# Performance work log

Measured on AMD Instinct MI355X. Metric: run time of the kernel, lower is better.

## Reference

```python
import jax, jax.numpy as jnp
import numpy as np

B, S, H, D = 4, 2048, 16, 128
E = H * D  # emb_dim = 2048


def setup_inputs() -> dict:
    key = jax.random.key(0)
    ks = jax.random.split(key, 9)
    s_in = 1.0 / np.sqrt(E)
    return {
        "inputs": jax.random.normal(ks[0], (B, S, E), dtype=jnp.float32),
        "Wq": jax.random.normal(ks[1], (E, E), dtype=jnp.float32) * s_in,
        "bq": jnp.zeros((E,), dtype=jnp.float32),
        "Wk": jax.random.normal(ks[2], (E, E), dtype=jnp.float32) * s_in,
        "bk": jnp.zeros((E,), dtype=jnp.float32),
        "Wv": jax.random.normal(ks[3], (E, E), dtype=jnp.float32) * s_in,
        "bv": jnp.zeros((E,), dtype=jnp.float32),
        "Wo": jax.random.normal(ks[4], (E, E), dtype=jnp.float32) * s_in,
        "bo": jnp.zeros((E,), dtype=jnp.float32),
    }


def reference(inputs, Wq, bq, Wk, bk, Wv, bv, Wo, bo):
    b, s, e = inputs.shape
    # QKV projections -> [B, H, S, D]
    q = (inputs @ Wq + bq).reshape(b, s, H, D).transpose(0, 2, 1, 3)
    k = (inputs @ Wk + bk).reshape(b, s, H, D).transpose(0, 2, 1, 3)
    v = (inputs @ Wv + bv).reshape(b, s, H, D).transpose(0, 2, 1, 3)
    scale = 1.0 / jnp.sqrt(jnp.asarray(D, dtype=q.dtype))
    # Scaled dot-product attention (what the blockwise flash loop computes)
    scores = jnp.einsum('bhqd,bhkd->bhqk', q, k) * scale
    probs = jax.nn.softmax(scores, axis=-1)
    attn = jnp.einsum('bhqk,bhkd->bhqd', probs, v)
    attn = attn.transpose(0, 2, 1, 3).reshape(b, s, e)
    return attn @ Wo + bo
```

## Files before the change

kernel.cpp:

```cpp
#include <hip/hip_runtime.h>
#include <hip/hip_bf16.h>
#include <stdint.h>

typedef __bf16 bf16;
typedef float f32x4 __attribute__((ext_vector_type(4)));
typedef bf16 bf16x4 __attribute__((ext_vector_type(4)));
typedef bf16 bf16x8 __attribute__((ext_vector_type(8)));

#define DEV __device__ __forceinline__

DEV void gload16(const void* g, void* l) {
  __builtin_amdgcn_global_load_lds((const __attribute__((address_space(1))) void*)g,
                                   (__attribute__((address_space(3))) void*)l, 16, 0, 0);
}

DEV f32x4 mfma16(bf16x8 a, bf16x8 b, f32x4 c) {
  return __builtin_amdgcn_mfma_f32_16x16x32_bf16(a, b, c, 0, 0, 0);
}

#if __has_builtin(__builtin_amdgcn_exp2f)
DEV float EXP2F(float x) { return __builtin_amdgcn_exp2f(x); }
#else
DEV float EXP2F(float x) { return exp2f(x); }
#endif

static constexpr int Bn = 4, Sn = 2048, Hn = 16, Dn = 128, En = 2048, Mn = 8192;

__global__ void prep(const float* __restrict__ X, bf16* __restrict__ Xb,
                     const float* __restrict__ Wq, const float* __restrict__ Wk,
                     const float* __restrict__ Wv, const float* __restrict__ Wo,
                     bf16* __restrict__ Wqt, bf16* __restrict__ Wkt,
                     bf16* __restrict__ Wvt, bf16* __restrict__ Wot, int n8) {
  __shared__ bf16 t[64][65];
  const int bid = blockIdx.x;
  if (bid < 2048) {
    int i = bid * 256 + threadIdx.x;
    const int stride = 2048 * 256;
    for (int idx = i; idx < n8; idx += stride) {
      const float4* p = (const float4*)(X + (size_t)idx * 8);
      float4 a = p[0], b = p[1];
      bf16x8 o;
      o[0]=(bf16)a.x; o[1]=(bf16)a.y; o[2]=(bf16)a.z; o[3]=(bf16)a.w;
      o[4]=(bf16)b.x; o[5]=(bf16)b.y; o[6]=(bf16)b.z; o[7]=(bf16)b.w;
      *(bf16x8*)(Xb + (size_t)idx * 8) = o;
    }
    return;
  }
  const int q = bid - 2048;
  const int mtx = q >> 10, within = q & 1023;
  const float* W = (mtx == 0) ? Wq : (mtx == 1) ? Wk : (mtx == 2) ? Wv : Wo;
  bf16* Wt = (mtx == 0) ? Wqt : (mtx == 1) ? Wkt : (mtx == 2) ? Wvt : Wot;
  int tx = threadIdx.x & 15, ty = threadIdx.x >> 4;
  int c0 = (within & 31) * 64, r0 = (within >> 5) * 64;
  #pragma unroll
  for (int i = 0; i < 4; ++i) {
    int r = i * 16 + ty;
    float4 v = *(const float4*)&W[(size_t)(r0 + r) * En + c0 + tx * 4];
    t[r][tx*4+0] = (bf16)v.x; t[r][tx*4+1] = (bf16)v.y;
    t[r][tx*4+2] = (bf16)v.z; t[r][tx*4+3] = (bf16)v.w;
  }
  __syncthreads();
  #pragma unroll
  for (int i = 0; i < 4; ++i) {
    int c = i * 16 + ty;
    bf16x4 o;
    #pragma unroll
    for (int j = 0; j < 4; ++j) o[j] = t[tx*4+j][c];
    *(bf16x4*)&Wt[(size_t)(c0 + c) * En + r0 + tx * 4] = o;
  }
}

#define STAGE_A(H, DBUF, KTN) do { \
    const bf16* s_ = A + (size_t)(mbase + (tid >> 2)) * K + (KTN) * 64 + (H) * 32 \
                     + (((tid & 3) ^ ((tid >> 3) & 3)) * 8); \
    gload16(s_, (DBUF) + (H) * 16384 + (w << 10)); \
  } while (0)
#define STAGE_B(H, DBUF, KTN) do { \
    const bf16* s_ = Bt + (size_t)(nbase + (tid >> 2)) * K + (KTN) * 64 + (H) * 32 \
                     + (((tid & 3) ^ ((tid >> 3) & 3)) * 8); \
    gload16(s_, (DBUF) + (H) * 16384 + (w << 10)); \
  } while (0)

template<int OUT_MODE>
__global__ __launch_bounds__(1024, 2) void gemm256(
    const bf16* __restrict__ A, const bf16* __restrict__ Bt,
    const float* __restrict__ b0, const float* __restrict__ b1,
    const float* __restrict__ b2, void* __restrict__ Cout,
    bf16* __restrict__ Vout,
    int M, int N, int K, int sbx, int sby)
{
  __shared__ __align__(16) uint8_t smem[131072];
  const int tid = threadIdx.x, lane = tid & 63, w = tid >> 6;
  const int wm = w >> 2, wn = w & 3;
  const int g = lane >> 4, lr = lane & 15;
  const int gx = (g ^ ((lr >> 1) & 3)) << 4;
  const int lid = blockIdx.x;
  const int xcd = lid & 7, i = lid >> 3;
  const int bx = (xcd & 1) * sbx + (i % sbx);
  const int by = (xcd >> 1) * sby + (i / sbx);
  const int mbase = by * 256, nbase = bx * 256;

  f32x4 acc[4][4] = {};

  STAGE_A(0, smem, 0);
  STAGE_B(0, smem + 65536, 0);
  STAGE_A(1, smem, 0);
  STAGE_B(1, smem + 65536, 0);
  asm volatile("s_waitcnt vmcnt(0)" ::: "memory");
  __builtin_amdgcn_s_barrier();

  const int NKT = K >> 6;
  for (int kt = 0; kt < NKT; ++kt) {
    const int cur = kt & 1;
    uint8_t* Acur = smem + (cur << 15);
    uint8_t* Bcur = smem + 65536 + (cur << 15);
    uint8_t* Anxt = smem + ((cur ^ 1) << 15);
    uint8_t* Bnxt = smem + 65536 + ((cur ^ 1) << 15);
    const bool notlast = (kt + 1 < NKT);

    if (notlast) {
      STAGE_A(0, Anxt, kt + 1);
      STAGE_B(0, Bnxt, kt + 1);
      STAGE_A(1, Anxt, kt + 1);
      STAGE_B(1, Bnxt, kt + 1);
    }

    #pragma unroll
    for (int kh = 0; kh < 2; ++kh) {
      bf16x8 af[4], bfv[4];
      #pragma unroll
      for (int mf = 0; mf < 4; ++mf)
        af[mf] = *(const bf16x8*)(Acur + kh * 16384 + (wm * 64 + mf * 16 + lr) * 64 + gx);
      #pragma unroll
      for (int j = 0; j < 4; ++j)
        bfv[j] = *(const bf16x8*)(Bcur + kh * 16384 + (wn * 64 + j * 16 + lr) * 64 + gx);
      __builtin_amdgcn_s_setprio(1);
      #pragma unroll
      for (int mf = 0; mf < 4; ++mf)
        #pragma unroll
        for (int j = 0; j < 4; ++j)
          acc[mf][j] = mfma16(af[mf], bfv[j], acc[mf][j]);
      __builtin_amdgcn_s_setprio(0);
    }

    asm volatile("s_waitcnt vmcnt(0)" ::: "memory");
    __builtin_amdgcn_s_barrier();
  }

  if constexpr (OUT_MODE == 0) {
    int tsel = nbase >> 11;
    if (tsel == 2) {
      #pragma unroll
      for (int j = 0; j < 4; ++j) {
        int nn = (nbase + wn * 64 + j * 16 + lr) & 2047;
        int h = nn >> 7, d = nn & 127;
        float bv = b2[nn];
        #pragma unroll
        for (int mf = 0; mf < 4; ++mf) {
          int m0 = mbase + wm * 64 + mf * 16 + g * 4;
          int b = m0 >> 11, s0 = m0 & 2047;
          bf16x4 o4;
          #pragma unroll
          for (int r = 0; r < 4; ++r) o4[r] = (bf16)(acc[mf][j][r] + bv);
          *(bf16x4*)&Vout[((size_t)(b * Hn + h) * Dn + d) * Sn + s0] = o4;
        }
      }
    } else {
      const float* bsel = (tsel == 0) ? b0 : b1;
      #pragma unroll
      for (int j = 0; j < 4; ++j) {
        int n = nbase + wn * 64 + j * 16 + lr;
        int nn = n & 2047;
        float bv = bsel[nn];
        int h = nn >> 7, d = nn & 127;
        #pragma unroll
        for (int mf = 0; mf < 4; ++mf) {
          #pragma unroll
          for (int r = 0; r < 4; ++r) {
            int m = mbase + wm * 64 + mf * 16 + g * 4 + r;
            int b = m >> 11, s = m & 2047;
            ((bf16*)Cout)[(size_t)tsel * ((size_t)Mn * En) +
                          ((size_t)(b * Hn + h) * Sn + s) * Dn + d] = (bf16)(acc[mf][j][r] + bv);
          }
        }
      }
    }
  } else {
    #pragma unroll
    for (int j = 0; j < 4; ++j) {
      int n = nbase + wn * 64 + j * 16 + lr;
      float bv = b0[n];
      #pragma unroll
      for (int mf = 0; mf < 4; ++mf) {
        #pragma unroll
        for (int r = 0; r < 4; ++r) {
          int m = mbase + wm * 64 + mf * 16 + g * 4 + r;
          ((float*)Cout)[(size_t)m * N + n] = acc[mf][j][r] + bv;
        }
      }
    }
  }
}

__global__ __launch_bounds__(512, 2) void attn(
    const bf16* __restrict__ Q, const bf16* __restrict__ K,
    const bf16* __restrict__ Vt, bf16* __restrict__ O)
{
  __shared__ __align__(16) uint8_t smem[65536];
  const int tid = threadIdx.x, lane = tid & 63, w = tid >> 6;
  const int g = lane >> 4, lr = lane & 15;
  const int lid = blockIdx.x;
  const int xcd = lid & 7, j = lid >> 3;
  const int bh = xcd * 8 + (j >> 3);
  const int q0 = (j & 7) * 256;
  const size_t hoff = (size_t)bh * Sn * Dn;
  const bf16* Qh = Q + hoff;
  const bf16* Kh = K + hoff;
  const bf16* Vh = Vt + hoff;
  const float SC2 = 0.12751744f;

  #pragma unroll
  for (int it = 0; it < 8; ++it) {
    int cl = it * 512 + tid;
    int row = cl >> 4, cs = cl & 15;
    int cg = cs ^ (row & 7);
    gload16(Qh + (size_t)(q0 + row) * Dn + cg * 8, smem + (it * 512 + (tid & ~63)) * 16);
  }
  __syncthreads();
  bf16x8 qf[2][4];
  #pragma unroll
  for (int nf = 0; nf < 2; ++nf)
    #pragma unroll
    for (int ks = 0; ks < 4; ++ks) {
      int row = w * 32 + nf * 16 + lr;
      qf[nf][ks] = *(const bf16x8*)(smem + row * 256 + (((ks * 4 + g) ^ (row & 7)) << 4));
    }
  __syncthreads();

  const int vd = tid >> 2, vq = tid & 3;
  const bf16* vrow = Vh + (size_t)vd * Sn + (vq >> 1) * 32 + (vq & 1) * 8;

  uint4 u0, u1;
  #pragma unroll
  for (int it = 0; it < 2; ++it) {
    int cl = it * 512 + tid;
    int row = cl >> 4, cs = cl & 15;
    int cg = cs ^ (row & 7);
    gload16(Kh + (size_t)row * Dn + cg * 8, smem + (it * 512 + (tid & ~63)) * 16);
  }
  { const uint4* vs = (const uint4*)vrow; u0 = vs[0]; u1 = vs[2]; }

  f32x4 o[2][8] = {};
  float m2[2] = { -__builtin_inff(), -__builtin_inff() };
  float lrun[2] = { 0.f, 0.f };

  for (int t = 0; t < 32; ++t) {
    const int cur = t & 1;
    uint8_t* Kcur = smem + (cur << 14);
    uint8_t* Knxt = smem + ((cur ^ 1) << 14);
    uint8_t* Vcur = smem + 32768 + (cur << 14);
    asm volatile("s_waitcnt vmcnt(0)" ::: "memory");
    {
      uint8_t* base = Vcur + vd * 128;
      const int sw = vd & 7;
      *(uint4*)(base + (((2 * vq + 0) ^ sw) << 4)) = make_uint4(u0.x, u0.y, u1.x, u1.y);
      *(uint4*)(base + (((2 * vq + 1) ^ sw) << 4)) = make_uint4(u0.z, u0.w, u1.z, u1.w);
    }
    if (t < 31) {
      const int kvn = (t + 1) * 64;
      #pragma unroll
      for (int it = 0; it < 2; ++it) {
        int cl = it * 512 + tid;
        int row = cl >> 4, cs = cl & 15;
        int cg = cs ^ (row & 7);
        gload16(Kh + (size_t)(kvn + row) * Dn + cg * 8,
                Knxt + (it * 512 + (tid & ~63)) * 16);
      }
      const uint4* vs = (const uint4*)(vrow + kvn);
      u0 = vs[0]; u1 = vs[2];
    }
    asm volatile("s_waitcnt lgkmcnt(0)" ::: "memory");
    asm volatile("s_barrier" ::: "memory");

    f32x4 sfr[2][4] = {};
    __builtin_amdgcn_s_setprio(1);
    #pragma unroll
    for (int ks = 0; ks < 4; ++ks) {
      #pragma unroll
      for (int mf = 0; mf < 4; ++mf) {
        int row = mf * 16 + lr;
        bf16x8 kf = *(const bf16x8*)(Kcur + row * 256 + (((ks * 4 + g) ^ (row & 7)) << 4));
        sfr[0][mf] = mfma16(kf, qf[0][ks], sfr[0][mf]);
        sfr[1][mf] = mfma16(kf, qf[1][ks], sfr[1][mf]);
      }
    }
    __builtin_amdgcn_s_setprio(0);

    bf16x8 pa[2][2];
    #pragma unroll
    for (int nf = 0; nf < 2; ++nf) {
      f32x4 a0, a1;
      #pragma unroll
      for (int r = 0; r < 4; ++r) a0[r] = fmaxf(sfr[nf][0][r], sfr[nf][1][r]);
      #pragma unroll
      for (int r = 0; r < 4; ++r) a1[r] = fmaxf(sfr[nf][2][r], sfr[nf][3][r]);
      #pragma unroll
      for (int r = 0; r < 4; ++r) a0[r] = fmaxf(a0[r], a1[r]);
      float mx = fmaxf(fmaxf(a0[0], a0[1]), fmaxf(a0[2], a0[3]));
      mx = fmaxf(mx, __shfl_xor(mx, 16));
      mx = fmaxf(mx, __shfl_xor(mx, 32));
      float pm2 = mx * SC2;
      if (__any(pm2 > m2[nf] + 8.f)) {
        float mnew = fmaxf(m2[nf], pm2);
        float fsc = EXP2F(m2[nf] - mnew);
        m2[nf] = mnew;
        lrun[nf] *= fsc;
        float fv[4];
        #pragma unroll
        for (int r = 0; r < 4; ++r) fv[r] = __shfl(fsc, g * 4 + r);
        #pragma unroll
        for (int df = 0; df < 8; ++df)
          #pragma unroll
          for (int r = 0; r < 4; ++r) o[nf][df][r] *= fv[r];
      }
      const float mc = m2[nf];
      f32x4 p[4];
      #pragma unroll
      for (int mf = 0; mf < 4; ++mf)
        #pragma unroll
        for (int r = 0; r < 4; ++r)
          p[mf][r] = EXP2F(__builtin_fmaf(sfr[nf][mf][r], SC2, -mc));
      f32x4 s0, s1;
      #pragma unroll
      for (int r = 0; r < 4; ++r) s0[r] = p[0][r] + p[1][r];
      #pragma unroll
      for (int r = 0; r < 4; ++r) s1[r] = p[2][r] + p[3][r];
      #pragma unroll
      for (int r = 0; r < 4; ++r) s0[r] += s1[r];
      float ps = (s0[0] + s0[1]) + (s0[2] + s0[3]);
      ps += __shfl_xor(ps, 16);
      ps += __shfl_xor(ps, 32);
      lrun[nf] += ps;
      #pragma unroll
      for (int ks = 0; ks < 2; ++ks) {
        bf16x8 tt;
        #pragma unroll
        for (int i = 0; i < 4; ++i) {
          tt[i]     = (bf16)p[2 * ks][i];
          tt[i + 4] = (bf16)p[2 * ks + 1][i];
        }
        pa[nf][ks] = tt;
      }
    }

    __builtin_amdgcn_s_setprio(1);
    #pragma unroll
    for (int ks = 0; ks < 2; ++ks) {
      #pragma unroll
      for (int df = 0; df < 8; ++df) {
        int row = df * 16 + lr;
        bf16x8 vf = *(const bf16x8*)(Vcur + row * 128 + (((ks * 4 + g) ^ (row & 7)) << 4));
        o[0][df] = mfma16(pa[0][ks], vf, o[0][df]);
        o[1][df] = mfma16(pa[1][ks], vf, o[1][df]);
      }
    }
    __builtin_amdgcn_s_setprio(0);
    asm volatile("s_barrier" ::: "memory");
  }

  const int b = bh >> 4, h = bh & 15;
  #pragma unroll
  for (int nf = 0; nf < 2; ++nf) {
    float inv = 1.f / lrun[nf];
    float iv[4];
    #pragma unroll
    for (int r = 0; r < 4; ++r) iv[r] = __shfl(inv, g * 4 + r);
    #pragma unroll
    for (int df = 0; df < 8; ++df) {
      #pragma unroll
      for (int r = 0; r < 4; ++r) {
        int qrow = q0 + w * 32 + nf * 16 + g * 4 + r;
        int d = df * 16 + lr;
        size_t m = (size_t)b * Sn + qrow;
        O[m * En + h * Dn + d] = (bf16)(o[nf][df][r] * iv[r]);
      }
    }
  }
}

extern "C" void kernel_launch(void* const* d_in, const int* in_sizes, int n_in,
                              void* d_out, int out_size, void* d_ws, size_t ws_size,
                              hipStream_t stream) {
  const float* X  = (const float*)d_in[0];
  const float* Wq = (const float*)d_in[1];
  const float* bq = (const float*)d_in[2];
  const float* Wk = (const float*)d_in[3];
  const float* bk = (const float*)d_in[4];
  const float* Wv = (const float*)d_in[5];
  const float* bv = (const float*)d_in[6];
  const float* Wo = (const float*)d_in[7];
  const float* bo = (const float*)d_in[8];

  bf16* ws = (bf16*)d_ws;
  const size_t szE = (size_t)Mn * En;
  const size_t szW = (size_t)En * En;
  bf16* Xb  = ws;
  bf16* Wqt = Xb + szE;
  bf16* Wkt = Wqt + szW;
  bf16* Wvt = Wkt + szW;
  bf16* Wot = Wvt + szW;
  bf16* Qb  = Wot + szW;
  bf16* Kb  = Qb + szE;
  bf16* Vb  = Kb + szE;
  bf16* Vtp = Vb + szE;
  bf16* AO  = Vb;

  prep<<<6144, 256, 0, stream>>>(X, Xb, Wq, Wk, Wv, Wo, Wqt, Wkt, Wvt, Wot,
                                 (int)(szE / 8));
  gemm256<0><<<768, 1024, 0, stream>>>(Xb, Wqt, bq, bk, bv, Qb, Vtp,
                                       Mn, 3 * En, En, 12, 8);
  attn<<<512, 512, 0, stream>>>(Qb, Kb, Vtp, AO);
  gemm256<1><<<256, 1024, 0, stream>>>(AO, Wot, bo, nullptr, nullptr, d_out, nullptr,
                                       Mn, En, En, 4, 8);
}
```

Measured before the change: 455.1 us.

## Load GEMM A operand directly to registers, stage only B in LDS

The GEMM kernel no longer stages the A tile through shared memory. Each wave loads its A fragments straight from global memory into registers, prefetching the next k-tile into a second register set. Only B stays double-buffered in LDS, which halves LDS use to 64KB. This removes LDS write/read traffic for A and frees shared memory, but adds register pressure and gives up cross-wave sharing of A (the 4 waves with the same wm each load the same A rows separately), raising global/L2 traffic.

Measured after the change: 1.485 ms. +226.3%, slower.

```diff
diff --git a/kernel.cpp b/kernel.cpp
--- a/kernel.cpp
+++ b/kernel.cpp
@@ -70,11 +70,6 @@
   }
 }
 
-#define STAGE_A(H, DBUF, KTN) do { \
-    const bf16* s_ = A + (size_t)(mbase + (tid >> 2)) * K + (KTN) * 64 + (H) * 32 \
-                     + (((tid & 3) ^ ((tid >> 3) & 3)) * 8); \
-    gload16(s_, (DBUF) + (H) * 16384 + (w << 10)); \
-  } while (0)
 #define STAGE_B(H, DBUF, KTN) do { \
     const bf16* s_ = Bt + (size_t)(nbase + (tid >> 2)) * K + (KTN) * 64 + (H) * 32 \
                      + (((tid & 3) ^ ((tid >> 3) & 3)) * 8); \
@@ -89,7 +84,7 @@
     bf16* __restrict__ Vout,
     int M, int N, int K, int sbx, int sby)
 {
-  __shared__ __align__(16) uint8_t smem[131072];
+  __shared__ __align__(16) uint8_t smem[65536];
   const int tid = threadIdx.x, lane = tid & 63, w = tid >> 6;
   const int wm = w >> 2, wn = w & 3;
   const int g = lane >> 4, lr = lane & 15;
@@ -100,37 +95,40 @@
   const int by = (xcd >> 1) * sby + (i / sbx);
   const int mbase = by * 256, nbase = bx * 256;
 
+  const bf16* Abase = A + (size_t)(mbase + wm * 64 + lr) * K + g * 8;
+  const size_t rstride = (size_t)16 * K;
+
   f32x4 acc[4][4] = {};
 
-  STAGE_A(0, smem, 0);
-  STAGE_B(0, smem + 65536, 0);
-  STAGE_A(1, smem, 0);
-  STAGE_B(1, smem + 65536, 0);
+  bf16x8 aP[8];
+  #pragma unroll
+  for (int u = 0; u < 8; ++u)
+    aP[u] = *(const bf16x8*)(Abase + (u & 3) * rstride + (u >> 2) * 32);
+  STAGE_B(0, smem, 0);
+  STAGE_B(1, smem, 0);
   asm volatile("s_waitcnt vmcnt(0)" ::: "memory");
   __builtin_amdgcn_s_barrier();
 
   const int NKT = K >> 6;
   for (int kt = 0; kt < NKT; ++kt) {
     const int cur = kt & 1;
-    uint8_t* Acur = smem + (cur << 15);
-    uint8_t* Bcur = smem + 65536 + (cur << 15);
-    uint8_t* Anxt = smem + ((cur ^ 1) << 15);
-    uint8_t* Bnxt = smem + 65536 + ((cur ^ 1) << 15);
+    uint8_t* Bcur = smem + (cur << 15);
+    uint8_t* Bnxt = smem + ((cur ^ 1) << 15);
     const bool notlast = (kt + 1 < NKT);
 
+    bf16x8 aN[8];
     if (notlast) {
-      STAGE_A(0, Anxt, kt + 1);
+      const bf16* An = Abase + (size_t)(kt + 1) * 64;
+      #pragma unroll
+      for (int u = 0; u < 8; ++u)
+        aN[u] = *(const bf16x8*)(An + (u & 3) * rstride + (u >> 2) * 32);
       STAGE_B(0, Bnxt, kt + 1);
-      STAGE_A(1, Anxt, kt + 1);
       STAGE_B(1, Bnxt, kt + 1);
     }
 
     #pragma unroll
     for (int kh = 0; kh < 2; ++kh) {
-      bf16x8 af[4], bfv[4];
-      #pragma unroll
-      for (int mf = 0; mf < 4; ++mf)
-        af[mf] = *(const bf16x8*)(Acur + kh * 16384 + (wm * 64 + mf * 16 + lr) * 64 + gx);
+      bf16x8 bfv[4];
       #pragma unroll
       for (int j = 0; j < 4; ++j)
         bfv[j] = *(const bf16x8*)(Bcur + kh * 16384 + (wn * 64 + j * 16 + lr) * 64 + gx);
@@ -139,12 +137,17 @@
       for (int mf = 0; mf < 4; ++mf)
         #pragma unroll
         for (int j = 0; j < 4; ++j)
-          acc[mf][j] = mfma16(af[mf], bfv[j], acc[mf][j]);
+          acc[mf][j] = mfma16(aP[kh * 4 + mf], bfv[j], acc[mf][j]);
       __builtin_amdgcn_s_setprio(0);
     }
 
     asm volatile("s_waitcnt vmcnt(0)" ::: "memory");
     __builtin_amdgcn_s_barrier();
+
+    if (notlast) {
+      #pragma unroll
+      for (int u = 0; u < 8; ++u) aP[u] = aN[u];
+    }
   }
 
   if constexpr (OUT_MODE == 0) {
```

## Use 4-slot ring of 32-wide K tiles with prefetch distance two in GEMM

Applied to the files above, without the earlier changes.

Replaces the double-buffered 64-wide K tile pipeline in the 256x256 GEMM with a four-slot ring of 32-wide K tiles. Loads are issued two tiles ahead, and the wait uses vmcnt(2) so one tile's loads stay in flight across the barrier. The goal is to hide global-to-LDS latency better. The cost is twice as many barriers per K and less MFMA work between them.

After: 471.2 us. 1.04x slower.

```diff
diff --git a/kernel.cpp b/kernel.cpp
--- a/kernel.cpp
+++ b/kernel.cpp
@@ -70,16 +70,14 @@
   }
 }
 
-#define STAGE_A(H, DBUF, KTN) do { \
-    const bf16* s_ = A + (size_t)(mbase + (tid >> 2)) * K + (KTN) * 64 + (H) * 32 \
-                     + (((tid & 3) ^ ((tid >> 3) & 3)) * 8); \
-    gload16(s_, (DBUF) + (H) * 16384 + (w << 10)); \
-  } while (0)
-#define STAGE_B(H, DBUF, KTN) do { \
-    const bf16* s_ = Bt + (size_t)(nbase + (tid >> 2)) * K + (KTN) * 64 + (H) * 32 \
-                     + (((tid & 3) ^ ((tid >> 3) & 3)) * 8); \
-    gload16(s_, (DBUF) + (H) * 16384 + (w << 10)); \
-  } while (0)
+#define STAGE_A(KTN) gload16( \
+    A + (size_t)(mbase + (tid >> 2)) * K + (KTN) * 32 \
+      + (((tid & 3) ^ ((tid >> 3) & 3)) * 8), \
+    smem + (((KTN) & 3) << 14) + tid * 16)
+#define STAGE_B(KTN) gload16( \
+    Bt + (size_t)(nbase + (tid >> 2)) * K + (KTN) * 32 \
+      + (((tid & 3) ^ ((tid >> 3) & 3)) * 8), \
+    smem + 65536 + (((KTN) & 3) << 14) + tid * 16)
 
 template<int OUT_MODE>
 __global__ __launch_bounds__(1024, 2) void gemm256(
@@ -102,48 +100,36 @@
 
   f32x4 acc[4][4] = {};
 
-  STAGE_A(0, smem, 0);
-  STAGE_B(0, smem + 65536, 0);
-  STAGE_A(1, smem, 0);
-  STAGE_B(1, smem + 65536, 0);
-  asm volatile("s_waitcnt vmcnt(0)" ::: "memory");
+  STAGE_A(0); STAGE_B(0);
+  STAGE_A(1); STAGE_B(1);
+  asm volatile("s_waitcnt vmcnt(2)" ::: "memory");
   __builtin_amdgcn_s_barrier();
 
-  const int NKT = K >> 6;
+  const int NKT = K >> 5;
   for (int kt = 0; kt < NKT; ++kt) {
-    const int cur = kt & 1;
-    uint8_t* Acur = smem + (cur << 15);
-    uint8_t* Bcur = smem + 65536 + (cur << 15);
-    uint8_t* Anxt = smem + ((cur ^ 1) << 15);
-    uint8_t* Bnxt = smem + 65536 + ((cur ^ 1) << 15);
-    const bool notlast = (kt + 1 < NKT);
-
-    if (notlast) {
-      STAGE_A(0, Anxt, kt + 1);
-      STAGE_B(0, Bnxt, kt + 1);
-      STAGE_A(1, Anxt, kt + 1);
-      STAGE_B(1, Bnxt, kt + 1);
-    }
-
-    #pragma unroll
-    for (int kh = 0; kh < 2; ++kh) {
-      bf16x8 af[4], bfv[4];
-      #pragma unroll
-      for (int mf = 0; mf < 4; ++mf)
-        af[mf] = *(const bf16x8*)(Acur + kh * 16384 + (wm * 64 + mf * 16 + lr) * 64 + gx);
+    uint8_t* Acur = smem + ((kt & 3) << 14);
+    uint8_t* Bcur = smem + 65536 + ((kt & 3) << 14);
+    const bool deep = (kt + 2 < NKT);
+
+    if (deep) { STAGE_A(kt + 2); STAGE_B(kt + 2); }
+
+    bf16x8 af[4], bfv[4];
+    #pragma unroll
+    for (int mf = 0; mf < 4; ++mf)
+      af[mf] = *(const bf16x8*)(Acur + (wm * 64 + mf * 16 + lr) * 64 + gx);
+    #pragma unroll
+    for (int j = 0; j < 4; ++j)
+      bfv[j] = *(const bf16x8*)(Bcur + (wn * 64 + j * 16 + lr) * 64 + gx);
+    __builtin_amdgcn_s_setprio(1);
+    #pragma unroll
+    for (int mf = 0; mf < 4; ++mf)
       #pragma unroll
       for (int j = 0; j < 4; ++j)
-        bfv[j] = *(const bf16x8*)(Bcur + kh * 16384 + (wn * 64 + j * 16 + lr) * 64 + gx);
-      __builtin_amdgcn_s_setprio(1);
-      #pragma unroll
-      for (int mf = 0; mf < 4; ++mf)
-        #pragma unroll
-        for (int j = 0; j < 4; ++j)
-          acc[mf][j] = mfma16(af[mf], bfv[j], acc[mf][j]);
-      __builtin_amdgcn_s_setprio(0);
-    }
-
-    asm volatile("s_waitcnt vmcnt(0)" ::: "memory");
+        acc[mf][j] = mfma16(af[mf], bfv[j], acc[mf][j]);
+    __builtin_amdgcn_s_setprio(0);
+
+    if (deep) { asm volatile("s_waitcnt vmcnt(2)" ::: "memory"); }
+    else      { asm volatile("s_waitcnt vmcnt(0)" ::: "memory"); }
     __builtin_amdgcn_s_barrier();
   }
 
```
